# Kernel tuning notes

Hardware: AMD Instinct MI355X
Metric: run time of the kernel (lower is better)

## Reference

```python
import jax, jax.numpy as jnp
import numpy as np

N_QUBITS = 4
N_LAYERS = 3
BATCH = 1048576  # 2**20; batched state vector [B, 2,2,2,2] complex64 = 128 MB


def setup_inputs() -> dict:
    key = jax.random.key(0)
    k1, k2 = jax.random.split(key)
    x = jax.random.normal(k1, (BATCH, N_QUBITS), dtype=jnp.float32)
    q_weights = jax.random.normal(k2, (N_LAYERS, N_QUBITS, 3), dtype=jnp.float32) * 0.1
    return {"x": x, "q_weights": q_weights}


def _ry_mat(theta):
    # RY(t) = [[cos t/2, -sin t/2], [sin t/2, cos t/2]]; theta: [] or [B]
    c = jnp.cos(theta * 0.5).astype(jnp.complex64)
    s = jnp.sin(theta * 0.5).astype(jnp.complex64)
    return jnp.stack([jnp.stack([c, -s], -1), jnp.stack([s, c], -1)], -2)


def _rz_mat(theta):
    # RZ(t) = diag(e^{-it/2}, e^{it/2})
    e = jnp.exp(-0.5j * theta.astype(jnp.complex64))
    z = jnp.zeros_like(e)
    return jnp.stack([jnp.stack([e, z], -1), jnp.stack([z, jnp.conj(e)], -1)], -2)


def _apply_1q(state, U, wire):
    # state: [B,2,2,2,2]; U: [2,2] (shared) or [B,2,2] (per-sample)
    ax = wire + 1
    state = jnp.moveaxis(state, ax, -1)
    if U.ndim == 3:
        state = jnp.einsum('b...o,bno->b...n', state, U)
    else:
        state = jnp.einsum('b...o,no->b...n', state, U)
    return jnp.moveaxis(state, -1, ax)


def _cnot(state, c, t):
    # flip target bit on the control=1 slice
    ca, ta = c + 1, t + 1
    s0 = jnp.take(state, 0, axis=ca)
    s1 = jnp.take(state, 1, axis=ca)
    ta2 = ta if ta < ca else ta - 1
    s1 = jnp.flip(s1, axis=ta2)
    return jnp.stack([s0, s1], axis=ca)


def _circuit(x, q_weights):
    B = x.shape[0]
    xn = jnp.tanh(x) * jnp.pi  # [B, 4]
    # |0000>
    state = jnp.zeros((B,) + (2,) * N_QUBITS, dtype=jnp.complex64)
    state = state.at[:, 0, 0, 0, 0].set(1.0 + 0.0j)
    # angle encoding: RY(2x_i) then RZ(x_i), per-sample batched 2x2 gates
    for i in range(N_QUBITS):
        state = _apply_1q(state, _ry_mat(2.0 * xn[:, i]), i)
        state = _apply_1q(state, _rz_mat(xn[:, i]), i)
    # variational layers: Rot(phi,theta,omega) = RZ(omega) @ RY(theta) @ RZ(phi)
    for l in range(N_LAYERS):
        for i in range(N_QUBITS):
            phi, theta, omega = q_weights[l, i, 0], q_weights[l, i, 1], q_weights[l, i, 2]
            U = _rz_mat(omega) @ _ry_mat(theta) @ _rz_mat(phi)
            state = _apply_1q(state, U, i)
        for i in range(N_QUBITS):
            state = _cnot(state, i, (i + 1) % N_QUBITS)
    # <Z_i> = p(bit_i=0) - p(bit_i=1)
    probs = jnp.abs(state) ** 2  # [B,2,2,2,2] real
    evs = []
    for i in range(N_QUBITS):
        axes = tuple(a for a in range(1, N_QUBITS + 1) if a != i + 1)
        marg = jnp.sum(probs, axis=axes)  # [B, 2]
        evs.append(marg[:, 0] - marg[:, 1])
    return jnp.stack(evs, axis=-1).astype(jnp.float32)  # [B, 4]


def reference(x, q_weights):
    return _circuit(x, q_weights)
```

## Files before the change

kernel.cpp:

```cpp
#include <hip/hip_runtime.h>


using f16x8  = __attribute__((ext_vector_type(8))) _Float16;
using f32x16 = __attribute__((ext_vector_type(16))) float;

struct C { float r, i; };

__device__ __forceinline__ C cmul(C a, C b) {
    C o;
    o.r = fmaf(a.r, b.r, -(a.i * b.i));
    o.i = fmaf(a.r, b.i,   a.i * b.r);
    return o;
}

__device__ __forceinline__ C cmadd(float ur, float ui, float wr, float wi, C a, C b) {
    C o;
    o.r = fmaf(ur, a.r, fmaf(-ui, a.i, fmaf(wr, b.r, -(wi * b.i))));
    o.i = fmaf(ur, a.i, fmaf( ui, a.r, fmaf(wr, b.i,   wi * b.r)));
    return o;
}

template <int BP>
__device__ __forceinline__ void apply_gate(C st[16], float4 A4, float4 B4) {
#pragma unroll
    for (int i = 0; i < 8; i++) {
        const int lo = ((i >> BP) << (BP + 1)) | (i & ((1 << BP) - 1));
        const int hi = lo | (1 << BP);
        const C a = st[lo], b = st[hi];
        st[lo] = cmadd(A4.x, A4.y, A4.z, A4.w, a, b);
        st[hi] = cmadd(B4.x, B4.y, B4.z, B4.w, a, b);
    }
}

template <int CB, int TB>
__device__ __forceinline__ void cnot(C st[16]) {
#pragma unroll
    for (int i = 0; i < 16; i++) {
        if ((i & (1 << CB)) && !(i & (1 << TB))) {
            C t = st[i];
            st[i] = st[i | (1 << TB)];
            st[i | (1 << TB)] = t;
        }
    }
}

struct Enc { float r0, i0, r1, i1; };
__device__ __forceinline__ Enc encode(float xq) {
    const float ax = fabsf(xq);
    const float e  = __builtin_amdgcn_exp2f(ax * -2.8853900817779268f);
    const float r  = __builtin_amdgcn_rcpf(1.0f + e);
    const float t  = copysignf((1.0f - e) * r, xq);
    const float sh = __builtin_amdgcn_sinf(t * 0.25f);
    const float ch = __builtin_amdgcn_cosf(t * 0.25f);
    const float s  = 2.0f * sh * ch;
    const float c  = fmaf(-2.0f * sh, sh, 1.0f);
    return {c * ch, -(c * sh), s * ch, s * sh};
}

__device__ __forceinline__ void wave_lds_fence() {
    asm volatile("s_waitcnt lgkmcnt(0)" ::: "memory");
    __builtin_amdgcn_sched_barrier(0);
}

#define WS_UG0 4096
#define ROWB 80

__global__ void qcompose_kernel(const float* __restrict__ qw, float* __restrict__ ws) {
    __shared__ float4 Ug[12][2];
    const int tid = threadIdx.x;
    if (tid < 12) {
        const float phi = qw[tid * 3 + 0];
        const float th  = qw[tid * 3 + 1];
        const float om  = qw[tid * 3 + 2];
        float s, c;   __sincosf(0.5f * th, &s, &c);
        float sa, ca; __sincosf(0.5f * (phi + om), &sa, &ca);
        float sb, cb; __sincosf(0.5f * (phi - om), &sb, &cb);
        Ug[tid][0] = make_float4(c * ca, -c * sa, -s * cb, -s * sb);
        Ug[tid][1] = make_float4(s * cb, -s * sb, c * ca, c * sa);
    }
    __syncthreads();

    if (tid < 4) {
        float4* o = reinterpret_cast<float4*>(reinterpret_cast<char*>(ws) + WS_UG0);
        o[2 * tid]     = Ug[tid][0];
        o[2 * tid + 1] = Ug[tid][1];
    }

    if (tid < 16) {
        C st[16];
#pragma unroll
        for (int i = 0; i < 16; i++) { st[i].r = 0.0f; st[i].i = 0.0f; }
        st[tid].r = 1.0f;

        cnot<3, 2>(st); cnot<2, 1>(st); cnot<1, 0>(st); cnot<0, 3>(st);
        apply_gate<3>(st, Ug[4][0], Ug[4][1]);
        apply_gate<2>(st, Ug[5][0], Ug[5][1]);
        apply_gate<1>(st, Ug[6][0], Ug[6][1]);
        apply_gate<0>(st, Ug[7][0], Ug[7][1]);
        cnot<3, 2>(st); cnot<2, 1>(st); cnot<1, 0>(st); cnot<0, 3>(st);
        apply_gate<3>(st, Ug[8][0], Ug[8][1]);
        apply_gate<2>(st, Ug[9][0], Ug[9][1]);
        apply_gate<1>(st, Ug[10][0], Ug[10][1]);
        apply_gate<0>(st, Ug[11][0], Ug[11][1]);
        cnot<3, 2>(st); cnot<2, 1>(st); cnot<1, 0>(st); cnot<0, 3>(st);

        _Float16* whi = reinterpret_cast<_Float16*>(ws);
        const int k0 = 2 * tid, k1 = k0 + 1;
#pragma unroll
        for (int d = 0; d < 16; d++) {
            const int j0 = 2 * d, j1 = j0 + 1;
            const float vr = st[d].r, vi = st[d].i;
            whi[j0 * 32 + k0] = (_Float16)vr;
            whi[j1 * 32 + k0] = (_Float16)vi;
            whi[j0 * 32 + k1] = (_Float16)(-vi);
            whi[j1 * 32 + k1] = (_Float16)vr;
        }
    }
}

__global__ __launch_bounds__(256, 8) void qlayer_kernel(const float* __restrict__ x,
                                                        const float* __restrict__ ws,
                                                        float* __restrict__ out, int B) {
    __shared__ __align__(16) unsigned char slab_all[4 * 64 * ROWB];
    const int tid  = threadIdx.x;
    const int lane = tid & 63;
    const int wid  = tid >> 6;
    char* slab  = reinterpret_cast<char*>(slab_all) + wid * (64 * ROWB);
    char* myrow = slab + lane * ROWB;

    const char* wsb = reinterpret_cast<const char*>(ws);

    const int j32 = lane & 31;
    const int h   = lane >> 5;
    const f16x8 Wh0 = *reinterpret_cast<const f16x8*>(wsb + j32 * 64 + h * 16);
    const f16x8 Wh1 = *reinterpret_cast<const f16x8*>(wsb + j32 * 64 + 32 + h * 16);
    const float4* ug0 = reinterpret_cast<const float4*>(wsb + WS_UG0);

    const int b  = blockIdx.x * 256 + tid;
    const int bl = (b < B) ? b : (B - 1);
    const float4 xv = reinterpret_cast<const float4*>(x)[bl];
    const float xs[4] = {xv.x, xv.y, xv.z, xv.w};

    C v[4][2];
#pragma unroll
    for (int q = 0; q < 4; q++) {
        const Enc e = encode(xs[q]);
        const C a{e.r0, e.i0}, bv{e.r1, e.i1};
        const float4 A4 = ug0[2 * q], B4 = ug0[2 * q + 1];
        v[q][0] = cmadd(A4.x, A4.y, A4.z, A4.w, a, bv);
        v[q][1] = cmadd(B4.x, B4.y, B4.z, B4.w, a, bv);
    }

    C t01[4], t23[4];
#pragma unroll
    for (int i = 0; i < 4; i++) {
        t01[i] = cmul(v[0][(i >> 1) & 1], v[1][i & 1]);
        t23[i] = cmul(v[2][(i >> 1) & 1], v[3][i & 1]);
    }
    f16x8 vh[4];
#pragma unroll
    for (int i = 0; i < 16; i++) {
        const C s = cmul(t01[i >> 2], t23[i & 3]);
        vh[i >> 2][2 * (i & 3)]     = (_Float16)s.r;
        vh[i >> 2][2 * (i & 3) + 1] = (_Float16)s.i;
    }
#pragma unroll
    for (int c = 0; c < 4; c++)
        *reinterpret_cast<f16x8*>(myrow + c * 16) = vh[c];

    wave_lds_fence();

    float r3[2], r2[2], r1[2], r0[2];
#pragma unroll
    for (int n = 0; n < 2; n++) {
        const char* srow = slab + (32 * n + j32) * ROWB + h * 16;
        const f16x8 S0 = *reinterpret_cast<const f16x8*>(srow);
        const f16x8 S1 = *reinterpret_cast<const f16x8*>(srow + 32);
        const f32x16 Z = {0.f,0.f,0.f,0.f,0.f,0.f,0.f,0.f,
                          0.f,0.f,0.f,0.f,0.f,0.f,0.f,0.f};
        f32x16 D = __builtin_amdgcn_mfma_f32_32x32x16_f16(Wh0, S0, Z, 0, 0, 0);
        D        = __builtin_amdgcn_mfma_f32_32x32x16_f16(Wh1, S1, D, 0, 0, 0);

        float p[8];
#pragma unroll
        for (int m = 0; m < 8; m++)
            p[m] = fmaf(D[2 * m + 1], D[2 * m + 1], D[2 * m] * D[2 * m]);

        const float e67 = p[6] + p[7];
        float t3 = (p[4] + p[5]) + e67;
        float t2 = (p[2] + p[3]) + e67;
        float t0 = (p[1] + p[3]) + (p[5] + p[7]);
        const float tAll = ((p[0] + p[2]) + (p[4] + p[6])) + t0;
        float t1 = h ? tAll : 0.0f;
        t3 += __shfl_xor(t3, 32); t2 += __shfl_xor(t2, 32);
        t1 += __shfl_xor(t1, 32); t0 += __shfl_xor(t0, 32);
        r3[n] = t3; r2[n] = t2; r1[n] = t1; r0[n] = t0;
    }
    const float e3 = h ? r3[1] : r3[0];
    const float e2 = h ? r2[1] : r2[0];
    const float e1 = h ? r1[1] : r1[0];
    const float e0 = h ? r0[1] : r0[0];

    if (b < B) {
        float4 ev;
        ev.x = fmaf(-2.0f, e3, 1.0f);
        ev.y = fmaf(-2.0f, e2, 1.0f);
        ev.z = fmaf(-2.0f, e1, 1.0f);
        ev.w = fmaf(-2.0f, e0, 1.0f);
        reinterpret_cast<float4*>(out)[b] = ev;
    }
}

extern "C" void kernel_launch(void* const* d_in, const int* in_sizes, int n_in,
                              void* d_out, int out_size, void* d_ws, size_t ws_size,
                              hipStream_t stream) {
    const float* x  = (const float*)d_in[0];
    const float* qw = (const float*)d_in[1];
    float* out = (float*)d_out;
    float* ws  = (float*)d_ws;
    const int B = in_sizes[0] / 4;
    const int blocks = (B + 255) / 256;
    qcompose_kernel<<<1, 64, 0, stream>>>(qw, ws);
    qlayer_kernel<<<blocks, 256, 0, stream>>>(x, ws, out, B);
}
```

Baseline: 79.97 us.

## Fold first variational layer into composed unitary and replace LDS staging with permlane32 swaps

Moves the first layer's Rot gates from per-sample work into the precomputed 16x16 unitary, so each sample only needs the encoding product state. The per-lane LDS write, wave fence and read-back used to build MFMA B operands is replaced by packed fp16 conversion plus permlane32_swap register exchanges. This cuts per-thread ALU work and LDS traffic and removes shared memory use, which may raise occupancy. The risk is that the swap lane mapping must exactly match the previous slab layout, and cvt_pkrtz rounds toward zero instead of to nearest.

```diff
diff --git a/kernel.cpp b/kernel.cpp
--- a/kernel.cpp
+++ b/kernel.cpp
@@ -2,7 +2,10 @@
 
 
 using f16x8  = __attribute__((ext_vector_type(8))) _Float16;
+using hf2    = __attribute__((ext_vector_type(2))) __fp16;
 using f32x16 = __attribute__((ext_vector_type(16))) float;
+using uint2v = __attribute__((ext_vector_type(2))) unsigned;
+using uint4v = __attribute__((ext_vector_type(4))) unsigned;
 
 struct C { float r, i; };
 
@@ -56,14 +59,6 @@
     const float c  = fmaf(-2.0f * sh, sh, 1.0f);
     return {c * ch, -(c * sh), s * ch, s * sh};
 }
-
-__device__ __forceinline__ void wave_lds_fence() {
-    asm volatile("s_waitcnt lgkmcnt(0)" ::: "memory");
-    __builtin_amdgcn_sched_barrier(0);
-}
-
-#define WS_UG0 4096
-#define ROWB 80
 
 __global__ void qcompose_kernel(const float* __restrict__ qw, float* __restrict__ ws) {
     __shared__ float4 Ug[12][2];
@@ -80,18 +75,16 @@
     }
     __syncthreads();
 
-    if (tid < 4) {
-        float4* o = reinterpret_cast<float4*>(reinterpret_cast<char*>(ws) + WS_UG0);
-        o[2 * tid]     = Ug[tid][0];
-        o[2 * tid + 1] = Ug[tid][1];
-    }
-
     if (tid < 16) {
         C st[16];
 #pragma unroll
         for (int i = 0; i < 16; i++) { st[i].r = 0.0f; st[i].i = 0.0f; }
         st[tid].r = 1.0f;
 
+        apply_gate<3>(st, Ug[0][0], Ug[0][1]);
+        apply_gate<2>(st, Ug[1][0], Ug[1][1]);
+        apply_gate<1>(st, Ug[2][0], Ug[2][1]);
+        apply_gate<0>(st, Ug[3][0], Ug[3][1]);
         cnot<3, 2>(st); cnot<2, 1>(st); cnot<1, 0>(st); cnot<0, 3>(st);
         apply_gate<3>(st, Ug[4][0], Ug[4][1]);
         apply_gate<2>(st, Ug[5][0], Ug[5][1]);
@@ -121,12 +114,8 @@
 __global__ __launch_bounds__(256, 8) void qlayer_kernel(const float* __restrict__ x,
                                                         const float* __restrict__ ws,
                                                         float* __restrict__ out, int B) {
-    __shared__ __align__(16) unsigned char slab_all[4 * 64 * ROWB];
     const int tid  = threadIdx.x;
     const int lane = tid & 63;
-    const int wid  = tid >> 6;
-    char* slab  = reinterpret_cast<char*>(slab_all) + wid * (64 * ROWB);
-    char* myrow = slab + lane * ROWB;
 
     const char* wsb = reinterpret_cast<const char*>(ws);
 
@@ -134,7 +123,6 @@
     const int h   = lane >> 5;
     const f16x8 Wh0 = *reinterpret_cast<const f16x8*>(wsb + j32 * 64 + h * 16);
     const f16x8 Wh1 = *reinterpret_cast<const f16x8*>(wsb + j32 * 64 + 32 + h * 16);
-    const float4* ug0 = reinterpret_cast<const float4*>(wsb + WS_UG0);
 
     const int b  = blockIdx.x * 256 + tid;
     const int bl = (b < B) ? b : (B - 1);
@@ -145,10 +133,8 @@
 #pragma unroll
     for (int q = 0; q < 4; q++) {
         const Enc e = encode(xs[q]);
-        const C a{e.r0, e.i0}, bv{e.r1, e.i1};
-        const float4 A4 = ug0[2 * q], B4 = ug0[2 * q + 1];
-        v[q][0] = cmadd(A4.x, A4.y, A4.z, A4.w, a, bv);
-        v[q][1] = cmadd(B4.x, B4.y, B4.z, B4.w, a, bv);
+        v[q][0] = C{e.r0, e.i0};
+        v[q][1] = C{e.r1, e.i1};
     }
 
     C t01[4], t23[4];
@@ -157,29 +143,41 @@
         t01[i] = cmul(v[0][(i >> 1) & 1], v[1][i & 1]);
         t23[i] = cmul(v[2][(i >> 1) & 1], v[3][i & 1]);
     }
-    f16x8 vh[4];
+    unsigned d[16];
 #pragma unroll
     for (int i = 0; i < 16; i++) {
         const C s = cmul(t01[i >> 2], t23[i & 3]);
-        vh[i >> 2][2 * (i & 3)]     = (_Float16)s.r;
-        vh[i >> 2][2 * (i & 3) + 1] = (_Float16)s.i;
-    }
-#pragma unroll
-    for (int c = 0; c < 4; c++)
-        *reinterpret_cast<f16x8*>(myrow + c * 16) = vh[c];
-
-    wave_lds_fence();
+        const hf2 pk = __builtin_amdgcn_cvt_pkrtz(s.r, s.i);
+        d[i] = __builtin_bit_cast(unsigned, pk);
+    }
+
+    unsigned f0a[4], f0b[4], f1a[4], f1b[4];
+#pragma unroll
+    for (int k = 0; k < 4; k++) {
+        const uint2v rA = __builtin_amdgcn_permlane32_swap(d[k],     d[4 + k],  false, false);
+        f0a[k] = rA.x;  f1a[k] = rA.y;
+        const uint2v rB = __builtin_amdgcn_permlane32_swap(d[8 + k], d[12 + k], false, false);
+        f0b[k] = rB.x;  f1b[k] = rB.y;
+    }
+    f16x8 S0v[2], S1v[2];
+    {
+        const uint4v a0 = {f0a[0], f0a[1], f0a[2], f0a[3]};
+        const uint4v b0 = {f0b[0], f0b[1], f0b[2], f0b[3]};
+        const uint4v a1 = {f1a[0], f1a[1], f1a[2], f1a[3]};
+        const uint4v b1 = {f1b[0], f1b[1], f1b[2], f1b[3]};
+        S0v[0] = __builtin_bit_cast(f16x8, a0);
+        S1v[0] = __builtin_bit_cast(f16x8, b0);
+        S0v[1] = __builtin_bit_cast(f16x8, a1);
+        S1v[1] = __builtin_bit_cast(f16x8, b1);
+    }
 
     float r3[2], r2[2], r1[2], r0[2];
 #pragma unroll
     for (int n = 0; n < 2; n++) {
-        const char* srow = slab + (32 * n + j32) * ROWB + h * 16;
-        const f16x8 S0 = *reinterpret_cast<const f16x8*>(srow);
-        const f16x8 S1 = *reinterpret_cast<const f16x8*>(srow + 32);
         const f32x16 Z = {0.f,0.f,0.f,0.f,0.f,0.f,0.f,0.f,
                           0.f,0.f,0.f,0.f,0.f,0.f,0.f,0.f};
-        f32x16 D = __builtin_amdgcn_mfma_f32_32x32x16_f16(Wh0, S0, Z, 0, 0, 0);
-        D        = __builtin_amdgcn_mfma_f32_32x32x16_f16(Wh1, S1, D, 0, 0, 0);
+        f32x16 D = __builtin_amdgcn_mfma_f32_32x32x16_f16(Wh0, S0v[n], Z, 0, 0, 0);
+        D        = __builtin_amdgcn_mfma_f32_32x32x16_f16(Wh1, S1v[n], D, 0, 0, 0);
 
         float p[8];
 #pragma unroll
```

Result: no change. 81.54 us (+2.0%).
